# Optimization experiments

Hardware: AMD Instinct MI355X
Metric: run time of the kernel (lower is better)

Reference implementation:

```python
import jax, jax.numpy as jnp
import numpy as np

EPS = 1e-5
RATIO = 8


def _conv3d(x, w, b, groups=1, pad=0):
    # x: [N,C,T,H,W], w: [O, C//groups, kT,kH,kW]
    y = jax.lax.conv_general_dilated(
        x, w, window_strides=(1, 1, 1), padding=[(pad, pad)] * 3,
        dimension_numbers=("NCDHW", "OIDHW", "NCDHW"), feature_group_count=groups)
    return y + b[None, :, None, None, None]


def _dwblock(x, pw1_w, pw1_b, dw_w, dw_b, pw2_w, pw2_b):
    # pointwise1 (1x1x1) -> depthwise 3x3x3 -> pointwise2 (1x1x1)
    mid = pw1_w.shape[0]
    x = _conv3d(x, pw1_w, pw1_b)
    x = _conv3d(x, dw_w, dw_b, groups=mid, pad=1)
    x = _conv3d(x, pw2_w, pw2_b)
    return x


def _make_dw_params(key, c_in, c_out, prefix):
    mid = c_in // RATIO
    ks = jax.random.split(key, 3)
    s = 0.02
    return {
        f"{prefix}_pw1_w": jax.random.normal(ks[0], (mid, c_in, 1, 1, 1), jnp.float32) * s,
        f"{prefix}_pw1_b": jnp.zeros((mid,), jnp.float32),
        f"{prefix}_dw_w": jax.random.normal(ks[1], (mid, 1, 3, 3, 3), jnp.float32) * s,
        f"{prefix}_dw_b": jnp.zeros((mid,), jnp.float32),
        f"{prefix}_pw2_w": jax.random.normal(ks[2], (c_out, mid, 1, 1, 1), jnp.float32) * s,
        f"{prefix}_pw2_b": jnp.zeros((c_out,), jnp.float32),
    }


def setup_inputs() -> dict:
    key = jax.random.key(0)
    N, C, T, H, W = 4, 256, 16, 28, 28
    KC, VC = 128, 256
    k0, k1, k2, k3, k4 = jax.random.split(key, 5)
    inp = {"input_": jax.random.normal(k0, (N, C, T, H, W), jnp.float32)}
    inp.update(_make_dw_params(k1, C, KC, "k"))
    inp.update(_make_dw_params(k2, C, KC, "q"))
    inp.update(_make_dw_params(k3, C, VC, "v"))
    inp.update(_make_dw_params(k4, VC, C, "r"))
    return inp


HEAD_COUNT = 8


def reference(input_,
              k_pw1_w, k_pw1_b, k_dw_w, k_dw_b, k_pw2_w, k_pw2_b,
              q_pw1_w, q_pw1_b, q_dw_w, q_dw_b, q_pw2_w, q_pw2_b,
              v_pw1_w, v_pw1_b, v_dw_w, v_dw_b, v_pw2_w, v_pw2_b,
              r_pw1_w, r_pw1_b, r_dw_w, r_dw_b, r_pw2_w, r_pw2_b):
    n, c, t, h, w = input_.shape
    L = t * h * w
    Hc = HEAD_COUNT

    keys = _dwblock(input_, k_pw1_w, k_pw1_b, k_dw_w, k_dw_b, k_pw2_w, k_pw2_b)
    queries = _dwblock(input_, q_pw1_w, q_pw1_b, q_dw_w, q_dw_b, q_pw2_w, q_pw2_b)
    values = _dwblock(input_, v_pw1_w, v_pw1_b, v_dw_w, v_dw_b, v_pw2_w, v_pw2_b)

    kc = keys.shape[1]
    vc = values.shape[1]
    hk, hv = kc // Hc, vc // Hc

    # [n, heads, head_dim, L]
    K = keys.reshape(n, Hc, hk, L)
    Q = queries.reshape(n, Hc, hk, L)
    V = values.reshape(n, Hc, hv, L)

    K = jax.nn.softmax(K, axis=3)          # softmax over sequence (dim=2 in torch slice)
    Q = jax.nn.softmax(Q, axis=2)          # softmax over per-head key channels (dim=1)

    # context = K @ V^T : [n, heads, hk, hv]
    context = jnp.einsum("nhkl,nhvl->nhkv", K, V)
    # attended = context^T @ Q : [n, heads, hv, L]
    attended = jnp.einsum("nhkv,nhkl->nhvl", context, Q)
    aggregated = attended.reshape(n, vc, t, h, w)

    reproj = _dwblock(aggregated, r_pw1_w, r_pw1_b, r_dw_w, r_dw_b, r_pw2_w, r_pw2_b)
    x = reproj + input_
    # f.layer_norm(x, x.size()): normalize over the WHOLE tensor, no affine
    mu = jnp.mean(x)
    var = jnp.mean((x - mu) ** 2)
    return (x - mu) / jnp.sqrt(var + EPS)
```

## Files before the change

### kernel.cpp

```cpp
#include <hip/hip_runtime.h>
#include <cstddef>

#define NB   4
#define CIN  256
#define TT   16
#define HH   28
#define WW   28
#define LL   12544
#define MIDC 32
#define KCC  128
#define VCC  256
#define HC   8
#define HK   16
#define HV   32
#define CTXSPLIT 14
#define CTXSTR 544
#define EPSV 1e-5f

typedef __attribute__((ext_vector_type(8))) short bf16x8;
typedef __attribute__((ext_vector_type(8))) unsigned short u16x8;
typedef __attribute__((ext_vector_type(4))) float f32x4;
typedef __attribute__((ext_vector_type(4))) unsigned short u16x4;

__device__ __forceinline__ float b2f(unsigned short u) {
    return __builtin_bit_cast(float, ((unsigned int)u) << 16);
}
__device__ __forceinline__ unsigned short f2b(float f) {
    unsigned int u = __builtin_bit_cast(unsigned int, f);
    u += 0x7FFFu + ((u >> 16) & 1u);
    return (unsigned short)(u >> 16);
}

#define XTF_N_STRIDE 3211264ull
#define MID_SET_STRIDE 1605632ull

struct WconvA { const float* w1[4]; const float* w2[4]; };
struct Pw1M  { const short* wt[3]; const float* b[3]; unsigned short* out[3]; };
struct DwA   { const unsigned short* in[3]; const float* w[3]; const float* b[3]; unsigned short* out[3]; };
struct Pw2M  { const short* w2f; const unsigned short* d; const float* b[3]; unsigned short* out[3]; };

__global__ __launch_bounds__(256) void wconv_kernel(WconvA a, short* __restrict__ w1f,
                                                    short* __restrict__ w2f)
{
    const int g = blockIdx.x*256 + threadIdx.x;
    if (g < 4096) {
        const int L = g & 63, kap = (g >> 6) & 7, mt = (g >> 9) & 1, set = g >> 10;
        const int m = 16*mt + (L & 15);
        const int c0 = 32*kap + 8*(L >> 4);
        const float* wp = a.w1[set] + m*CIN + c0;
#pragma unroll
        for (int j = 0; j < 8; ++j) w1f[(size_t)g*8 + j] = (short)f2b(wp[j]);
    } else if (g < 4096 + 3072) {
        const int g2 = g - 4096;
        const int L = g2 & 63, mtg = g2 >> 6;
        int set, mtl;
        if (mtg < 8)       { set = 0; mtl = mtg; }
        else if (mtg < 16) { set = 1; mtl = mtg - 8; }
        else if (mtg < 32) { set = 2; mtl = mtg - 16; }
        else               { set = 3; mtl = mtg - 32; }
        const int m = 16*mtl + (L & 15);
        const int c0 = 8*(L >> 4);
        const float* wp = a.w2[set] + m*MIDC + c0;
#pragma unroll
        for (int j = 0; j < 8; ++j) w2f[(size_t)g2*8 + j] = (short)f2b(wp[j]);
    }
}

template<int NS>
__global__ __launch_bounds__(256) void pw1_direct(const float* __restrict__ in, Pw1M a)
{
    const int n = blockIdx.y, bx = blockIdx.x;
    const int t = threadIdx.x, wid = t >> 6, lane = t & 63;
    const int mt = wid & 1, lh = wid >> 1;
    const int tau0 = bx*8 + lh*4;
    const float* ib = in + (size_t)n*CIN*LL;
    const int colb = lane & 15, qq = lane >> 4;

    f32x4 acc[NS][4];
#pragma unroll
    for (int s = 0; s < NS; ++s)
#pragma unroll
        for (int i = 0; i < 4; ++i)
#pragma unroll
            for (int r = 0; r < 4; ++r) acc[s][i][r] = 0.f;

    for (int kap = 0; kap < 8; ++kap) {
        const int c0 = 32*kap + 8*qq;
        bf16x8 bfr[4];
#pragma unroll
        for (int i = 0; i < 4; ++i) {
            const float* p = ib + (size_t)c0*LL + (tau0 + i)*16 + colb;
#pragma unroll
            for (int j = 0; j < 8; ++j) bfr[i][j] = (short)f2b(p[(size_t)j*LL]);
        }
#pragma unroll
        for (int s = 0; s < NS; ++s) {
            bf16x8 afr = *reinterpret_cast<const bf16x8*>(
                a.wt[s] + ((mt*8 + kap)*512 + lane*8));
#pragma unroll
            for (int i = 0; i < 4; ++i)
                acc[s][i] = __builtin_amdgcn_mfma_f32_16x16x32_bf16(afr, bfr[i], acc[s][i], 0, 0, 0);
        }
    }
    const int m0 = mt*16 + qq*4;
#pragma unroll
    for (int s = 0; s < NS; ++s) {
        const float* bb = a.b[s];
        unsigned short* op = a.out[s] + (size_t)n*MIDC*LL;
#pragma unroll
        for (int r = 0; r < 4; ++r) {
            const float bv = bb[m0 + r];
#pragma unroll
            for (int i = 0; i < 4; ++i)
                op[(size_t)(m0 + r)*LL + (tau0 + i)*16 + colb] = f2b(acc[s][i][r] + bv);
        }
    }
}

__global__ __launch_bounds__(256) void pw1_frag(const short* __restrict__ xtf, Pw1M a)
{
    const int n = blockIdx.y, bx = blockIdx.x;
    const int t = threadIdx.x, wid = t >> 6, lane = t & 63;
    const int mt = wid & 1, lh = wid >> 1;
    const int tau0 = bx*8 + lh*4;
    const short* xb = xtf + (size_t)n*XTF_N_STRIDE;

    f32x4 acc[4];
#pragma unroll
    for (int i = 0; i < 4; ++i)
#pragma unroll
        for (int r = 0; r < 4; ++r) acc[i][r] = 0.f;

    for (int kap = 0; kap < 8; ++kap) {
        bf16x8 afr = *reinterpret_cast<const bf16x8*>(a.wt[0] + ((mt*8 + kap)*512 + lane*8));
#pragma unroll
        for (int i = 0; i < 4; ++i) {
            bf16x8 bfr = *reinterpret_cast<const bf16x8*>(
                xb + ((size_t)((tau0 + i)*8 + kap)*512 + lane*8));
            acc[i] = __builtin_amdgcn_mfma_f32_16x16x32_bf16(afr, bfr, acc[i], 0, 0, 0);
        }
    }
    const float* bb = a.b[0];
    unsigned short* op = a.out[0] + (size_t)n*MIDC*LL;
    const int col = lane & 15;
    const int m0 = mt*16 + (lane >> 4)*4;
#pragma unroll
    for (int r = 0; r < 4; ++r) {
        const float bv = bb[m0 + r];
#pragma unroll
        for (int i = 0; i < 4; ++i)
            op[(size_t)(m0 + r)*LL + (tau0 + i)*16 + col] = f2b(acc[i][r] + bv);
    }
}

struct Row6 { float v[6]; };

__device__ __forceinline__ Row6 load_row(const unsigned short* base, int zz, int yy, int x0)
{
    Row6 r;
    const bool ok = (zz >= 0) && (zz < TT) && (yy >= 0) && (yy < HH);
    if (ok) {
        const unsigned short* p = base + zz*(HH*WW) + yy*WW + x0;
        u16x4 m4 = *reinterpret_cast<const u16x4*>(p);
        r.v[0] = (x0 > 0)  ? b2f(p[-1]) : 0.f;
        r.v[1] = b2f(m4[0]); r.v[2] = b2f(m4[1]);
        r.v[3] = b2f(m4[2]); r.v[4] = b2f(m4[3]);
        r.v[5] = (x0 < 24) ? b2f(p[4]) : 0.f;
    } else {
#pragma unroll
        for (int i = 0; i < 6; ++i) r.v[i] = 0.f;
    }
    return r;
}

__device__ __forceinline__ void acc9(float& a0, float& a1, float& a2, float& a3,
                                     const Row6* rows, const float* w9)
{
#pragma unroll
    for (int dy = 0; dy < 3; ++dy)
#pragma unroll
        for (int dx = 0; dx < 3; ++dx) {
            const float wv = w9[dy*3 + dx];
            a0 = fmaf(wv, rows[dy].v[0 + dx], a0);
            a1 = fmaf(wv, rows[dy].v[1 + dx], a1);
            a2 = fmaf(wv, rows[dy].v[2 + dx], a2);
            a3 = fmaf(wv, rows[dy].v[3 + dx], a3);
        }
}

__global__ __launch_bounds__(256) void dw_reg(DwA a)
{
    const int tid = threadIdx.x;
    if (tid >= 196) return;
    const int z  = blockIdx.z;
    const int nm = blockIdx.y;
    const int m  = nm & (MIDC-1);
    const int t0 = blockIdx.x * 8;

    const float* wp = a.w[z] + m*27;
    float wv[27];
#pragma unroll
    for (int i = 0; i < 27; ++i) wv[i] = wp[i];
    const float bias = a.b[z][m];

    const int xg = tid % 7, y = tid / 7;
    const int x0 = xg*4;
    const unsigned short* ip = a.in[z] + (size_t)nm*LL;
    unsigned short* op = a.out[z] + (size_t)nm*LL;

    Row6 win[3][3];
#pragma unroll
    for (int dy = 0; dy < 3; ++dy) {
        win[0][dy] = load_row(ip, t0-1, y+dy-1, x0);
        win[1][dy] = load_row(ip, t0,   y+dy-1, x0);
    }
#pragma unroll
    for (int tt = 0; tt < 8; ++tt) {
        const int p0 = tt % 3, p1 = (tt+1) % 3, p2 = (tt+2) % 3;
        const int znew = t0 + tt + 1;
        win[p2][0] = load_row(ip, znew, y-1, x0);
        win[p2][1] = load_row(ip, znew, y,   x0);
        win[p2][2] = load_row(ip, znew, y+1, x0);

        float a0 = bias, a1 = bias, a2 = bias, a3 = bias;
        acc9(a0, a1, a2, a3, win[p0], wv);
        acc9(a0, a1, a2, a3, win[p1], wv + 9);
        acc9(a0, a1, a2, a3, win[p2], wv + 18);

        u16x4 o4 = { f2b(a0), f2b(a1), f2b(a2), f2b(a3) };
        *reinterpret_cast<u16x4*>(op + (size_t)(t0+tt)*(HH*WW) + y*WW + x0) = o4;
    }
}

__global__ __launch_bounds__(256) void pw2_g(Pw2M a)
{
    const int z = blockIdx.z, n = blockIdx.y, bx = blockIdx.x;
    int set, chunk;
    if (z < 2)      { set = 0; chunk = z; }
    else if (z < 4) { set = 1; chunk = z - 2; }
    else            { set = 2; chunk = z - 4; }
    const int OC   = (set == 2) ? 256 : 128;
    const int off2 = (set == 0) ? 0 : (set == 1) ? 8 : 16;

    const int t = threadIdx.x, wid = t >> 6, lane = t & 63;
    const int mtile = chunk*4 + wid;
    bf16x8 afr = *reinterpret_cast<const bf16x8*>(
        a.w2f + ((size_t)(off2 + mtile)*512 + lane*8));
    const unsigned short* db = a.d + (size_t)set*MID_SET_STRIDE + (size_t)n*MIDC*LL;
    const int colb = lane & 15, c0 = 8*(lane >> 4);

    f32x4 acc[4];
#pragma unroll
    for (int i = 0; i < 4; ++i) {
#pragma unroll
        for (int r = 0; r < 4; ++r) acc[i][r] = 0.f;
        const unsigned short* p = db + (size_t)c0*LL + (bx*4 + i)*16 + colb;
        bf16x8 bfr;
#pragma unroll
        for (int j = 0; j < 8; ++j) bfr[j] = (short)p[(size_t)j*LL];
        acc[i] = __builtin_amdgcn_mfma_f32_16x16x32_bf16(afr, bfr, acc[i], 0, 0, 0);
    }
    const float* bb = a.b[set];
    unsigned short* op = a.out[set] + (size_t)n*OC*LL;
    const int m0 = 16*mtile + (lane >> 4)*4;
#pragma unroll
    for (int r = 0; r < 4; ++r) {
        const float bv = bb[m0 + r];
#pragma unroll
        for (int i = 0; i < 4; ++i)
            op[(size_t)(m0 + r)*LL + (bx*4 + i)*16 + colb] = f2b(acc[i][r] + bv);
    }
}

__global__ __launch_bounds__(256) void ctx_mfma(
    const unsigned short* __restrict__ Kb, const unsigned short* __restrict__ Vb,
    float* __restrict__ ctxp)
{
    const int nh = blockIdx.y;
    const int sp = blockIdx.x;
    const int n = nh >> 3, h = nh & 7;
    const int t = threadIdx.x, w = t >> 6, lane = t & 63;
    const int i = lane & 15, q = lane >> 4;

    const unsigned short* Kp = Kb + ((size_t)(n*KCC + h*HK))*LL;
    const unsigned short* Vp = Vb + ((size_t)(n*VCC + h*HV))*LL;

    f32x4 a0 = {0.f,0.f,0.f,0.f}, a1 = {0.f,0.f,0.f,0.f};
    float asum = 0.f;

    const int cbase = sp*28 + w*7;
#pragma unroll 2
    for (int cc = 0; cc < 7; ++cc) {
        const int l0 = (cbase + cc)*32 + 8*q;
        bf16x8 kf = *reinterpret_cast<const bf16x8*>(Kp + (size_t)i*LL + l0);
        bf16x8 pf;
#pragma unroll
        for (int j = 0; j < 8; ++j) {
            const float e = __expf(b2f((unsigned short)kf[j]));
            asum += e;
            pf[j] = (short)f2b(e);
        }
        bf16x8 b0 = *reinterpret_cast<const bf16x8*>(Vp + (size_t)i*LL + l0);
        bf16x8 b1 = *reinterpret_cast<const bf16x8*>(Vp + (size_t)(i+16)*LL + l0);
        a0 = __builtin_amdgcn_mfma_f32_16x16x32_bf16(pf, b0, a0, 0, 0, 0);
        a1 = __builtin_amdgcn_mfma_f32_16x16x32_bf16(pf, b1, a1, 0, 0, 0);
    }
    asum += __shfl_xor(asum, 16);
    asum += __shfl_xor(asum, 32);

    __shared__ float cs[4][512];
    __shared__ float as[4][16];
#pragma unroll
    for (int r = 0; r < 4; ++r) {
        cs[w][(q*4 + r)*32 + i]      = a0[r];
        cs[w][(q*4 + r)*32 + 16 + i] = a1[r];
    }
    if (q == 0) as[w][i] = asum;
    __syncthreads();
    float* cp = ctxp + ((size_t)nh*CTXSPLIT + sp)*CTXSTR;
    for (int p = t; p < 512; p += 256)
        cp[p] = cs[0][p] + cs[1][p] + cs[2][p] + cs[3][p];
    if (t < 16) cp[512 + t] = as[0][t] + as[1][t] + as[2][t] + as[3][t];
}

__global__ void ctx_reduce(const float* __restrict__ ctxp, float* __restrict__ ctx)
{
    const int idx = blockIdx.x*256 + threadIdx.x;
    const int nh = idx >> 9;
    const int p  = idx & 511;
    const int k  = p >> 5;
    float s = 0.f, se = 0.f;
    for (int sp = 0; sp < CTXSPLIT; ++sp) {
        const float* cp = ctxp + ((size_t)nh*CTXSPLIT + sp)*CTXSTR;
        s  += cp[p];
        se += cp[512 + k];
    }
    ctx[idx] = s / se;
}

__global__ __launch_bounds__(256) void attended_kernel(
    const float* __restrict__ ctx, const unsigned short* __restrict__ Qb,
    short* __restrict__ aggf)
{
    const int nh = blockIdx.y;
    const int n = nh >> 3, h = nh & 7;
    const int l = blockIdx.x*256 + threadIdx.x;
    const float* __restrict__ cl = ctx + (size_t)nh*512;

    const unsigned short* Qp = Qb + ((size_t)(n*KCC + h*HK))*LL + l;
    float q[HK];
    float mx = -1e30f;
#pragma unroll
    for (int k = 0; k < HK; ++k) { q[k] = b2f(Qp[(size_t)k*LL]); mx = fmaxf(mx, q[k]); }
    float s = 0.f;
#pragma unroll
    for (int k = 0; k < HK; ++k) { q[k] = __expf(q[k] - mx); s += q[k]; }
    const float inv = 1.f / s;
#pragma unroll
    for (int k = 0; k < HK; ++k) q[k] *= inv;

    float av[HV];
#pragma unroll 4
    for (int v = 0; v < HV; ++v) {
        float acc = 0.f;
#pragma unroll
        for (int k = 0; k < HK; ++k) acc += q[k] * cl[k*HV + v];
        av[v] = acc;
    }
    short* ob = aggf + (size_t)n*XTF_N_STRIDE + ((size_t)((l >> 4)*8 + h))*512;
#pragma unroll
    for (int qd = 0; qd < 4; ++qd) {
        bf16x8 vv;
#pragma unroll
        for (int j = 0; j < 8; ++j) vv[j] = (short)f2b(av[qd*8 + j]);
        *reinterpret_cast<bf16x8*>(ob + (qd*16 + (l & 15))*8) = vv;
    }
}

__global__ __launch_bounds__(256) void pw2r_g(
    const unsigned short* __restrict__ d, const short* __restrict__ w2f,
    const float* __restrict__ bias, const float* __restrict__ resid,
    unsigned short* __restrict__ xout, float* __restrict__ part)
{
    const int z = blockIdx.z, n = blockIdx.y, bx = blockIdx.x;
    const int t = threadIdx.x, wid = t >> 6, lane = t & 63;
    const int mtile = z*4 + wid;
    bf16x8 afr = *reinterpret_cast<const bf16x8*>(
        w2f + ((size_t)(32 + mtile)*512 + lane*8));
    const unsigned short* db = d + (size_t)n*MIDC*LL;
    const int colb = lane & 15, c0 = 8*(lane >> 4);

    f32x4 acc[4];
#pragma unroll
    for (int i = 0; i < 4; ++i) {
#pragma unroll
        for (int r = 0; r < 4; ++r) acc[i][r] = 0.f;
        const unsigned short* p = db + (size_t)c0*LL + (bx*4 + i)*16 + colb;
        bf16x8 bfr;
#pragma unroll
        for (int j = 0; j < 8; ++j) bfr[j] = (short)p[(size_t)j*LL];
        acc[i] = __builtin_amdgcn_mfma_f32_16x16x32_bf16(afr, bfr, acc[i], 0, 0, 0);
    }
    const int m0 = 16*mtile + (lane >> 4)*4;
    float s1 = 0.f, s2 = 0.f;
#pragma unroll
    for (int r = 0; r < 4; ++r) {
        const float bv = bias[m0 + r];
#pragma unroll
        for (int i = 0; i < 4; ++i) {
            const size_t off = (size_t)(n*CIN + m0 + r)*LL + (bx*4 + i)*16 + colb;
            const float v = acc[i][r] + bv + resid[off];
            xout[off] = f2b(v);
            s1 += v; s2 += v*v;
        }
    }
    __shared__ float red[256];
    const int bid = (z*NB + n)*196 + bx;
    red[t] = s1; __syncthreads();
    for (int s = 128; s > 0; s >>= 1) { if (t < s) red[t] += red[t+s]; __syncthreads(); }
    if (t == 0) part[2*bid] = red[0];
    __syncthreads();
    red[t] = s2; __syncthreads();
    for (int s = 128; s > 0; s >>= 1) { if (t < s) red[t] += red[t+s]; __syncthreads(); }
    if (t == 0) part[2*bid + 1] = red[0];
}

__global__ void stats_kernel(const float* __restrict__ part, int nblocks,
                             float* __restrict__ stats)
{
    __shared__ float r1[256], r2[256];
    const int t = threadIdx.x;
    float s1 = 0.f, s2 = 0.f;
    for (int i = t; i < nblocks; i += 256) { s1 += part[2*i]; s2 += part[2*i+1]; }
    r1[t] = s1; r2[t] = s2; __syncthreads();
    for (int s = 128; s > 0; s >>= 1) { if (t < s) { r1[t] += r1[t+s]; r2[t] += r2[t+s]; } __syncthreads(); }
    if (t == 0) {
        const float M = (float)NB*CIN*LL;
        const float mu = r1[0]/M;
        const float var = r2[0]/M - mu*mu;
        stats[0] = mu;
        stats[1] = 1.0f/sqrtf(var + EPSV);
    }
}

__global__ __launch_bounds__(256) void norm_bf16(
    const unsigned short* __restrict__ x, const float* __restrict__ stats,
    float* __restrict__ out)
{
    const float mu = stats[0], inv = stats[1];
    const size_t total = (size_t)NB*CIN*LL;
    for (size_t i = ((size_t)blockIdx.x*256 + threadIdx.x)*8; i < total;
         i += (size_t)gridDim.x*256*8) {
        u16x8 v = *reinterpret_cast<const u16x8*>(x + i);
        float4 o0, o1;
        o0.x = (b2f(v[0])-mu)*inv; o0.y = (b2f(v[1])-mu)*inv;
        o0.z = (b2f(v[2])-mu)*inv; o0.w = (b2f(v[3])-mu)*inv;
        o1.x = (b2f(v[4])-mu)*inv; o1.y = (b2f(v[5])-mu)*inv;
        o1.z = (b2f(v[6])-mu)*inv; o1.w = (b2f(v[7])-mu)*inv;
        *reinterpret_cast<float4*>(out + i)     = o0;
        *reinterpret_cast<float4*>(out + i + 4) = o1;
    }
}

extern "C" void kernel_launch(void* const* d_in, const int* in_sizes, int n_in,
                              void* d_out, int out_size, void* d_ws, size_t ws_size,
                              hipStream_t stream) {
    const float* input   = (const float*)d_in[0];
    const float* k_pw1_w = (const float*)d_in[1];
    const float* k_pw1_b = (const float*)d_in[2];
    const float* k_dw_w  = (const float*)d_in[3];
    const float* k_dw_b  = (const float*)d_in[4];
    const float* k_pw2_w = (const float*)d_in[5];
    const float* k_pw2_b = (const float*)d_in[6];
    const float* q_pw1_w = (const float*)d_in[7];
    const float* q_pw1_b = (const float*)d_in[8];
    const float* q_dw_w  = (const float*)d_in[9];
    const float* q_dw_b  = (const float*)d_in[10];
    const float* q_pw2_w = (const float*)d_in[11];
    const float* q_pw2_b = (const float*)d_in[12];
    const float* v_pw1_w = (const float*)d_in[13];
    const float* v_pw1_b = (const float*)d_in[14];
    const float* v_dw_w  = (const float*)d_in[15];
    const float* v_dw_b  = (const float*)d_in[16];
    const float* v_pw2_w = (const float*)d_in[17];
    const float* v_pw2_b = (const float*)d_in[18];
    const float* r_pw1_w = (const float*)d_in[19];
    const float* r_pw1_b = (const float*)d_in[20];
    const float* r_dw_w  = (const float*)d_in[21];
    const float* r_dw_b  = (const float*)d_in[22];
    const float* r_pw2_w = (const float*)d_in[23];
    const float* r_pw2_b = (const float*)d_in[24];

    char* base = (char*)d_ws;
    unsigned short* dbuf = (unsigned short*)base;
    short* aggf = (short*)base;
    unsigned short* midb  = (unsigned short*)(base + 25690112);
    unsigned short* mid_r = midb;
    unsigned short* d_r   = (unsigned short*)(base + 25690112 + 6422528);
    unsigned short* Kb = (unsigned short*)(base + 54591488);
    unsigned short* Qb = (unsigned short*)(base + 67436544);
    unsigned short* Vb = (unsigned short*)(base + 80281600);
    unsigned short* xb = (unsigned short*)(base + 54591488);
    char* H = base + 105971712;
    float* ctxp   = (float*)H;
    float* ctx    = (float*)(H + 974848);
    float* part   = (float*)(H + 1040384);
    float* statsp = (float*)(H + 1065472);
    short* w1f    = (short*)(H + 1065536);
    short* w2f    = (short*)(H + 1131072);

    {
        WconvA a;
        a.w1[0]=k_pw1_w; a.w1[1]=q_pw1_w; a.w1[2]=v_pw1_w; a.w1[3]=r_pw1_w;
        a.w2[0]=k_pw2_w; a.w2[1]=q_pw2_w; a.w2[2]=v_pw2_w; a.w2[3]=r_pw2_w;
        wconv_kernel<<<28, 256, 0, stream>>>(a, w1f, w2f);
    }
    {
        Pw1M a;
        a.wt[0]=w1f;        a.wt[1]=w1f+8192;   a.wt[2]=w1f+16384;
        a.b[0]=k_pw1_b;     a.b[1]=q_pw1_b;     a.b[2]=v_pw1_b;
        a.out[0]=midb;      a.out[1]=midb+MID_SET_STRIDE; a.out[2]=midb+2*MID_SET_STRIDE;
        pw1_direct<3><<<dim3(98, NB), 256, 0, stream>>>(input, a);
    }
    {
        DwA a;
        a.in[0]=midb; a.in[1]=midb+MID_SET_STRIDE; a.in[2]=midb+2*MID_SET_STRIDE;
        a.w[0]=k_dw_w; a.w[1]=q_dw_w; a.w[2]=v_dw_w;
        a.b[0]=k_dw_b; a.b[1]=q_dw_b; a.b[2]=v_dw_b;
        a.out[0]=dbuf; a.out[1]=dbuf+MID_SET_STRIDE; a.out[2]=dbuf+2*MID_SET_STRIDE;
        dw_reg<<<dim3(2, NB*MIDC, 3), 256, 0, stream>>>(a);
    }
    {
        Pw2M a;
        a.w2f = w2f; a.d = dbuf;
        a.b[0]=k_pw2_b; a.b[1]=q_pw2_b; a.b[2]=v_pw2_b;
        a.out[0]=Kb; a.out[1]=Qb; a.out[2]=Vb;
        pw2_g<<<dim3(196, NB, 8), 256, 0, stream>>>(a);
    }
    ctx_mfma<<<dim3(CTXSPLIT, NB*HC), 256, 0, stream>>>(Kb, Vb, ctxp);
    ctx_reduce<<<64, 256, 0, stream>>>(ctxp, ctx);
    attended_kernel<<<dim3(49, NB*HC), 256, 0, stream>>>(ctx, Qb, aggf);
    {
        Pw1M a;
        a.wt[0]=w1f+24576; a.wt[1]=a.wt[0]; a.wt[2]=a.wt[0];
        a.b[0]=r_pw1_b;    a.b[1]=a.b[0];   a.b[2]=a.b[0];
        a.out[0]=mid_r;    a.out[1]=a.out[0]; a.out[2]=a.out[0];
        pw1_frag<<<dim3(98, NB), 256, 0, stream>>>(aggf, a);
    }
    {
        DwA a;
        a.in[0]=mid_r; a.w[0]=r_dw_w; a.b[0]=r_dw_b; a.out[0]=d_r;
        a.in[1]=a.in[0]; a.w[1]=a.w[0]; a.b[1]=a.b[0]; a.out[1]=a.out[0];
        a.in[2]=a.in[0]; a.w[2]=a.w[0]; a.b[2]=a.b[0]; a.out[2]=a.out[0];
        dw_reg<<<dim3(2, NB*MIDC, 1), 256, 0, stream>>>(a);
    }
    pw2r_g<<<dim3(196, NB, 4), 256, 0, stream>>>(d_r, w2f, r_pw2_b, input, xb, part);
    stats_kernel<<<1, 256, 0, stream>>>(part, 3136, statsp);
    norm_bf16<<<2048, 256, 0, stream>>>(xb, statsp, (float*)d_out);
}
```

Measured before the change: 143.7 us.

## Restructure pw1 so each wave covers both output M-tiles and one column tile

```diff
diff --git a/kernel.cpp b/kernel.cpp
--- a/kernel.cpp
+++ b/kernel.cpp
@@ -66,53 +66,48 @@
     }
 }
 
-template<int NS>
-__global__ __launch_bounds__(256) void pw1_direct(const float* __restrict__ in, Pw1M a)
-{
-    const int n = blockIdx.y, bx = blockIdx.x;
+__global__ __launch_bounds__(128) void pw1_direct2(const float* __restrict__ in, Pw1M a)
+{
+    const int n = blockIdx.y;
     const int t = threadIdx.x, wid = t >> 6, lane = t & 63;
-    const int mt = wid & 1, lh = wid >> 1;
-    const int tau0 = bx*8 + lh*4;
+    const int tau = blockIdx.x*2 + wid;
     const float* ib = in + (size_t)n*CIN*LL;
     const int colb = lane & 15, qq = lane >> 4;
 
-    f32x4 acc[NS][4];
-#pragma unroll
-    for (int s = 0; s < NS; ++s)
-#pragma unroll
-        for (int i = 0; i < 4; ++i)
-#pragma unroll
-            for (int r = 0; r < 4; ++r) acc[s][i][r] = 0.f;
+    f32x4 acc[3][2];
+#pragma unroll
+    for (int s = 0; s < 3; ++s)
+#pragma unroll
+        for (int mt = 0; mt < 2; ++mt)
+#pragma unroll
+            for (int r = 0; r < 4; ++r) acc[s][mt][r] = 0.f;
 
     for (int kap = 0; kap < 8; ++kap) {
         const int c0 = 32*kap + 8*qq;
-        bf16x8 bfr[4];
-#pragma unroll
-        for (int i = 0; i < 4; ++i) {
-            const float* p = ib + (size_t)c0*LL + (tau0 + i)*16 + colb;
-#pragma unroll
-            for (int j = 0; j < 8; ++j) bfr[i][j] = (short)f2b(p[(size_t)j*LL]);
+        const float* p = ib + (size_t)c0*LL + tau*16 + colb;
+        bf16x8 bfr;
+#pragma unroll
+        for (int j = 0; j < 8; ++j) bfr[j] = (short)f2b(p[(size_t)j*LL]);
+#pragma unroll
+        for (int s = 0; s < 3; ++s) {
+#pragma unroll
+            for (int mt = 0; mt < 2; ++mt) {
+                bf16x8 afr = *reinterpret_cast<const bf16x8*>(
+                    a.wt[s] + ((mt*8 + kap)*512 + lane*8));
+                acc[s][mt] = __builtin_amdgcn_mfma_f32_16x16x32_bf16(afr, bfr, acc[s][mt], 0, 0, 0);
+            }
         }
-#pragma unroll
-        for (int s = 0; s < NS; ++s) {
-            bf16x8 afr = *reinterpret_cast<const bf16x8*>(
-                a.wt[s] + ((mt*8 + kap)*512 + lane*8));
-#pragma unroll
-            for (int i = 0; i < 4; ++i)
-                acc[s][i] = __builtin_amdgcn_mfma_f32_16x16x32_bf16(afr, bfr[i], acc[s][i], 0, 0, 0);
-        }
-    }
-    const int m0 = mt*16 + qq*4;
-#pragma unroll
-    for (int s = 0; s < NS; ++s) {
+    }
+#pragma unroll
+    for (int s = 0; s < 3; ++s) {
         const float* bb = a.b[s];
         unsigned short* op = a.out[s] + (size_t)n*MIDC*LL;
 #pragma unroll
-        for (int r = 0; r < 4; ++r) {
-            const float bv = bb[m0 + r];
-#pragma unroll
-            for (int i = 0; i < 4; ++i)
-                op[(size_t)(m0 + r)*LL + (tau0 + i)*16 + colb] = f2b(acc[s][i][r] + bv);
+        for (int mt = 0; mt < 2; ++mt) {
+            const int m0 = mt*16 + qq*4;
+#pragma unroll
+            for (int r = 0; r < 4; ++r)
+                op[(size_t)(m0 + r)*LL + tau*16 + colb] = f2b(acc[s][mt][r] + bb[m0 + r]);
         }
     }
 }
@@ -520,7 +515,7 @@
         a.wt[0]=w1f;        a.wt[1]=w1f+8192;   a.wt[2]=w1f+16384;
         a.b[0]=k_pw1_b;     a.b[1]=q_pw1_b;     a.b[2]=v_pw1_b;
         a.out[0]=midb;      a.out[1]=midb+MID_SET_STRIDE; a.out[2]=midb+2*MID_SET_STRIDE;
-        pw1_direct<3><<<dim3(98, NB), 256, 0, stream>>>(input, a);
+        pw1_direct2<<<dim3(392, NB), 128, 0, stream>>>(input, a);
     }
     {
         DwA a;
```

Result: no change. 143.0 us (-0.5%).
